# Kernel optimization log

Hardware: AMD Instinct MI355X
Metric: run time of the kernel (lower is better)

Reference implementation:

```python
import jax, jax.numpy as jnp
import numpy as np

WS = 8        # window_size
SS = 4        # shift_size
NH = 8        # num_heads
DIM = 256
HD = DIM // NH
SCALE = HD ** -0.5
EPS = 1e-5


def _rel_pos_index(ws):
    ch, cw = np.meshgrid(np.arange(ws), np.arange(ws), indexing='ij')
    coords = np.stack([ch.ravel(), cw.ravel()])            # [2, ws*ws]
    rel = coords[:, :, None] - coords[:, None, :]           # [2, N, N]
    rel = rel.transpose(1, 2, 0)
    rel[:, :, 0] += ws - 1
    rel[:, :, 1] += ws - 1
    rel[:, :, 0] *= 2 * ws - 1
    return jnp.asarray(rel.sum(-1))                         # [N, N] int

REL_IDX = _rel_pos_index(WS)


def _ln(x, g, b):
    m = jnp.mean(x, axis=-1, keepdims=True)
    v = jnp.mean(jnp.square(x - m), axis=-1, keepdims=True)
    return (x - m) * jax.lax.rsqrt(v + EPS) * g + b


def setup_inputs() -> dict:
    key = jax.random.key(0)
    ks = jax.random.split(key, 12)
    B, L, C = 8, 16384, DIM
    s = lambda k, shape, scale=0.02: jax.random.normal(k, shape, jnp.float32) * scale
    return {
        'x': jax.random.normal(ks[0], (B, L, C), jnp.float32),
        'norm1_g': jnp.ones((C,), jnp.float32),
        'norm1_b': jnp.zeros((C,), jnp.float32),
        'qkv_w': s(ks[1], (C, 3 * C)),
        'qkv_b': jnp.zeros((3 * C,), jnp.float32),
        'rel_bias': s(ks[2], ((2 * WS - 1) ** 2, NH)),
        'proj_w': s(ks[3], (C, C)),
        'proj_b': jnp.zeros((C,), jnp.float32),
        'norm2_g': jnp.ones((C,), jnp.float32),
        'norm2_b': jnp.zeros((C,), jnp.float32),
        'fc1_w': s(ks[4], (C, C)),
        'fc1_b': jnp.zeros((C,), jnp.float32),
        'fc2_w': s(ks[5], (C, C)),
        'fc2_b': jnp.zeros((C,), jnp.float32),
        'H': 128,
        'W': 128,
    }


def reference(x, norm1_g, norm1_b, qkv_w, qkv_b, rel_bias, proj_w, proj_b,
              norm2_g, norm2_b, fc1_w, fc1_b, fc2_w, fc2_b, H, W):
    B, L, C = x.shape
    shortcut = x
    h = _ln(x, norm1_g, norm1_b).reshape(B, H, W, C)
    pad_b = (WS - H % WS) % WS
    pad_r = (WS - W % WS) % WS
    h = jnp.pad(h, ((0, 0), (0, pad_b), (0, pad_r), (0, 0)))
    Hp, Wp = H + pad_b, W + pad_r
    if SS > 0:
        h = jnp.roll(h, (-SS, -SS), axis=(1, 2))
    # window partition -> [B*nW, WS*WS, C]
    h = h.reshape(B, Hp // WS, WS, Wp // WS, WS, C)
    h = h.transpose(0, 1, 3, 2, 4, 5).reshape(-1, WS * WS, C)
    Bn, N = h.shape[0], WS * WS
    # attention
    qkv = (h @ qkv_w + qkv_b).reshape(Bn, N, 3, NH, HD)
    q, k, v = qkv[:, :, 0], qkv[:, :, 1], qkv[:, :, 2]   # [Bn, N, NH, HD]
    attn = jnp.einsum('bnhd,bmhd->bhnm', q * SCALE, k)
    bias = rel_bias[REL_IDX.reshape(-1)].reshape(N, N, NH).transpose(2, 0, 1)
    attn = jax.nn.softmax(attn + bias[None], axis=-1)
    o = jnp.einsum('bhnm,bmhd->bnhd', attn, v).reshape(Bn, N, C)
    o = o @ proj_w + proj_b
    # window reverse
    o = o.reshape(B, Hp // WS, Wp // WS, WS, WS, C)
    o = o.transpose(0, 1, 3, 2, 4, 5).reshape(B, Hp, Wp, C)
    if SS > 0:
        o = jnp.roll(o, (SS, SS), axis=(1, 2))
    o = o[:, :H, :W, :].reshape(B, H * W, C)
    x = shortcut + o
    # MLP (hidden = dim, exact GELU as nn.GELU default)
    m = _ln(x, norm2_g, norm2_b)
    m = jax.nn.gelu(m @ fc1_w + fc1_b, approximate=False)
    m = m @ fc2_w + fc2_b
    return x + m
```

## Files before the change

### kernel.cpp

```cpp
#include <hip/hip_runtime.h>
#include <stdint.h>

typedef __bf16 bf16;
typedef __bf16 bf16x4v __attribute__((ext_vector_type(4)));
typedef __bf16 bf16x8 __attribute__((ext_vector_type(8)));
typedef float floatx4 __attribute__((ext_vector_type(4)));
typedef float float4v __attribute__((ext_vector_type(4)));

#define SCALE 0.17677669529663689f

__device__ __forceinline__ float ldin(const void* p, long i, int f32) {
  return f32 ? ((const float*)p)[i] : (float)(((const bf16*)p)[i]);
}

__global__ void detect_k(const unsigned short* __restrict__ x, int* flag) {
  __shared__ int cnt;
  if (threadIdx.x == 0) cnt = 0;
  __syncthreads();
  int local = 0;
  for (int i = threadIdx.x; i < 4096; i += 256) {
    unsigned short w = x[i];
    int e = (w >> 7) & 0xFF;
    if (w != 0 && (e >= 0x9F || e <= 0x5F)) local++;
  }
  atomicAdd(&cnt, local);
  __syncthreads();
  if (threadIdx.x == 0) *flag = (cnt >= 64) ? 1 : 0;
}

__global__ void conv_w_k(const void* __restrict__ W, bf16* __restrict__ Wt,
                         int K, int N, const int* __restrict__ flag) {
  int f32 = *flag;
  int idx = blockIdx.x * 256 + threadIdx.x;
  if (idx < K * N) {
    int k = idx / N, n = idx % N;
    Wt[n * K + k] = (bf16)ldin(W, idx, f32);
  }
}

__global__ void bias_k(const void* __restrict__ rel, float* __restrict__ bias_s,
                       const int* __restrict__ flag) {
  int f = *flag;
  int idx = blockIdx.x * 256 + threadIdx.x;
  int r = idx & 3, ni = (idx >> 2) & 3, mi = (idx >> 4) & 3;
  int l16 = (idx >> 6) & 15, quad = (idx >> 10) & 3, head = idx >> 12;
  int i = mi * 16 + quad * 4 + r, j = ni * 16 + l16;
  int dy = (i >> 3) - (j >> 3) + 7, dx = (i & 7) - (j & 7) + 7;
  bias_s[idx] = ldin(rel, (dy * 15 + dx) * 8 + head, f);
}

__global__ __launch_bounds__(256) void ln_k(const void* __restrict__ x,
                                            const void* __restrict__ g,
                                            const void* __restrict__ b,
                                            bf16* __restrict__ y,
                                            const int* __restrict__ flag,
                                            int x_input) {
  int f = *flag;
  int f32x = x_input ? f : 0;
  int wave = threadIdx.x >> 6, lane = threadIdx.x & 63;
  long row = (long)blockIdx.x * 4 + wave;
  float v[4];
  if (f32x) {
    float4v u = ((const float4v*)x)[row * 64 + lane];
    for (int i = 0; i < 4; i++) v[i] = u[i];
  } else {
    bf16x4v u = ((const bf16x4v*)x)[row * 64 + lane];
    for (int i = 0; i < 4; i++) v[i] = (float)u[i];
  }
  float s = v[0] + v[1] + v[2] + v[3];
  for (int off = 32; off > 0; off >>= 1) s += __shfl_xor(s, off, 64);
  float mean = s * (1.f / 256.f);
  float q = 0.f;
  for (int i = 0; i < 4; i++) { float d = v[i] - mean; q += d * d; }
  for (int off = 32; off > 0; off >>= 1) q += __shfl_xor(q, off, 64);
  float rstd = rsqrtf(q * (1.f / 256.f) + 1e-5f);
  bf16x4v o;
  for (int i = 0; i < 4; i++) {
    float gv = ldin(g, lane * 4 + i, f);
    float bv = ldin(b, lane * 4 + i, f);
    o[i] = (bf16)((v[i] - mean) * rstd * gv + bv);
  }
  ((bf16x4v*)y)[row * 64 + lane] = o;
}

template <int EPI>
__global__ __launch_bounds__(256) void gemm_bt_k(
    const bf16* __restrict__ A, const bf16* __restrict__ Bt,
    const void* __restrict__ bias, const void* __restrict__ res,
    void* __restrict__ C, int M, int N, int K, const int* __restrict__ flag,
    int res_input, int out_input) {
  __shared__ bf16 As[128 * 32];
  __shared__ bf16 Bs[128 * 32];
  __shared__ float CsF[32 * 132];
  const int tid = threadIdx.x;
  const int ntiles = gridDim.x;
  int bid = blockIdx.y * ntiles + blockIdx.x;
  const int nwg = ntiles * gridDim.y;
  if (!(nwg & 7)) bid = (bid & 7) * (nwg >> 3) + (bid >> 3);
  const long m0 = (long)(bid / ntiles) * 128;
  const int n0 = (bid % ntiles) * 128;
  const int wave = tid >> 6, lane = tid & 63;
  const int wm = wave & 1, wn = wave >> 1;
  const int quad = lane >> 4, l16 = lane & 15;

  floatx4 acc[4][4];
  for (int i = 0; i < 4; i++)
    for (int j = 0; j < 4; j++) acc[i][j] = (floatx4){0.f, 0.f, 0.f, 0.f};

  const int ldr = tid >> 2;
  const int ldc = (tid & 3) * 8;

  for (int kt = 0; kt < K; kt += 32) {
    bf16x8 a0 = *(const bf16x8*)(A + (m0 + ldr) * K + kt + ldc);
    bf16x8 a1 = *(const bf16x8*)(A + (m0 + 64 + ldr) * K + kt + ldc);
    bf16x8 b0 = *(const bf16x8*)(Bt + (long)(n0 + ldr) * K + kt + ldc);
    bf16x8 b1 = *(const bf16x8*)(Bt + (long)(n0 + 64 + ldr) * K + kt + ldc);
    __syncthreads();
    *(bf16x8*)&As[tid * 8] = a0;
    *(bf16x8*)&As[(256 + tid) * 8] = a1;
    *(bf16x8*)&Bs[tid * 8] = b0;
    *(bf16x8*)&Bs[(256 + tid) * 8] = b1;
    __syncthreads();
    bf16x8 af[4], bfr[4];
    for (int mi = 0; mi < 4; mi++)
      af[mi] = *(const bf16x8*)&As[(wm * 64 + mi * 16 + l16) * 32 + quad * 8];
    for (int ni = 0; ni < 4; ni++)
      bfr[ni] = *(const bf16x8*)&Bs[(wn * 64 + ni * 16 + l16) * 32 + quad * 8];
    for (int mi = 0; mi < 4; mi++)
      for (int ni = 0; ni < 4; ni++)
        acc[mi][ni] = __builtin_amdgcn_mfma_f32_16x16x32_bf16(
            af[mi], bfr[ni], acc[mi][ni], 0, 0, 0);
  }

  const int f = *flag;
  const int rf32 = res_input ? f : 0;
  const int of32 = out_input ? f : 0;
  for (int mi = 0; mi < 4; mi++) {
    __syncthreads();
    for (int ni = 0; ni < 4; ni++) {
      int col = n0 + wn * 64 + ni * 16 + l16;
      float bv = ldin(bias, col, f);
      for (int r = 0; r < 4; r++) {
        long row = m0 + wm * 64 + mi * 16 + quad * 4 + r;
        float v = acc[mi][ni][r] + bv;
        if (EPI == 1) v = v * 0.5f * (1.f + erff(v * 0.70710678118654752f));
        if (EPI == 2) v += ldin(res, row * N + col, rf32);
        CsF[(wm * 16 + quad * 4 + r) * 132 + wn * 64 + ni * 16 + l16] = v;
      }
    }
    __syncthreads();
    const int s = tid >> 3;
    const int seg = tid & 7;
    const long grow = m0 + (s >> 4) * 64 + mi * 16 + (s & 15);
    const int gcol = n0 + seg * 16;
    const float4v* src = (const float4v*)&CsF[s * 132 + seg * 16];
    float4v v0 = src[0], v1 = src[1], v2 = src[2], v3 = src[3];
    if (of32) {
      float4v* dst = (float4v*)((float*)C + grow * N + gcol);
      dst[0] = v0; dst[1] = v1; dst[2] = v2; dst[3] = v3;
    } else {
      bf16x8 o0, o1;
      for (int j = 0; j < 4; j++) {
        o0[j] = (bf16)v0[j]; o0[4 + j] = (bf16)v1[j];
        o1[j] = (bf16)v2[j]; o1[4 + j] = (bf16)v3[j];
      }
      bf16x8* dst = (bf16x8*)((bf16*)C + grow * N + gcol);
      dst[0] = o0; dst[1] = o1;
    }
  }
}

__global__ __launch_bounds__(256) void attn_k(const bf16* __restrict__ qkv,
                                              const float* __restrict__ bias_s,
                                              bf16* __restrict__ o) {
  __shared__ bf16 Pb[4][64 * 64];
  __shared__ bf16 Vb[4][32 * 64];
  const int tid = threadIdx.x;
  const int wave = tid >> 6, lane = tid & 63;
  const int quad = lane >> 4, l16 = lane & 15;
  const int gid = blockIdx.x * 4 + wave;
  const int head = gid & 7, win = gid >> 3;
  const int wx = win & 15, wy = (win >> 4) & 15, bb = win >> 8;

  bf16* P = Pb[wave];
  bf16* Vt = Vb[wave];

  bf16x8 qf[4], kf[4];
  for (int mi = 0; mi < 4; mi++) {
    int t = mi * 16 + l16;
    int rr = (wy * 8 + (t >> 3) + 4) & 127;
    int cc = (wx * 8 + (t & 7) + 4) & 127;
    long base = ((long)(bb * 16384 + rr * 128 + cc)) * 768 + head * 32 + quad * 8;
    qf[mi] = *(const bf16x8*)(qkv + base);
    kf[mi] = *(const bf16x8*)(qkv + base + 256);
    bf16x8 vv = *(const bf16x8*)(qkv + base + 512);
    int tcol = t ^ (quad << 4);
    for (int jj = 0; jj < 8; jj++) Vt[(quad * 8 + jj) * 64 + tcol] = vv[jj];
  }
  __syncthreads();

  floatx4 acc[4][4];
  for (int mi = 0; mi < 4; mi++)
    for (int ni = 0; ni < 4; ni++) {
      floatx4 z = (floatx4){0.f, 0.f, 0.f, 0.f};
      acc[mi][ni] = __builtin_amdgcn_mfma_f32_16x16x32_bf16(qf[mi], kf[ni], z, 0, 0, 0);
    }

  const float4v* bp =
      (const float4v*)(bias_s + (((head * 4 + quad) * 16 + l16) << 6));
  for (int mi = 0; mi < 4; mi++) {
    float mx[4] = {-1e30f, -1e30f, -1e30f, -1e30f};
    for (int ni = 0; ni < 4; ni++) {
      float4v bv = bp[mi * 4 + ni];
      for (int r = 0; r < 4; r++) {
        acc[mi][ni][r] = acc[mi][ni][r] * SCALE + bv[r];
        mx[r] = fmaxf(mx[r], acc[mi][ni][r]);
      }
    }
    for (int r = 0; r < 4; r++) {
      float m = mx[r];
      for (int off = 1; off < 16; off <<= 1) m = fmaxf(m, __shfl_xor(m, off, 64));
      mx[r] = m;
    }
    float sm[4] = {0.f, 0.f, 0.f, 0.f};
    for (int ni = 0; ni < 4; ni++)
      for (int r = 0; r < 4; r++) {
        float e = __expf(acc[mi][ni][r] - mx[r]);
        acc[mi][ni][r] = e;
        sm[r] += e;
      }
    for (int r = 0; r < 4; r++) {
      float s = sm[r];
      for (int off = 1; off < 16; off <<= 1) s += __shfl_xor(s, off, 64);
      sm[r] = 1.f / s;
    }
    for (int ni = 0; ni < 4; ni++)
      for (int r = 0; r < 4; r++) {
        int i = mi * 16 + quad * 4 + r;
        int j = ni * 16 + l16;
        P[i * 64 + (j ^ ((i & 7) << 3))] = (bf16)(acc[mi][ni][r] * sm[r]);
      }
  }
  __syncthreads();

  floatx4 oacc[4][2];
  for (int mi = 0; mi < 4; mi++)
    for (int nt = 0; nt < 2; nt++) oacc[mi][nt] = (floatx4){0.f, 0.f, 0.f, 0.f};
  for (int ks = 0; ks < 2; ks++) {
    bf16x8 vfr[2];
    for (int nt = 0; nt < 2; nt++) {
      int d = nt * 16 + l16;
      vfr[nt] =
          *(const bf16x8*)&Vt[d * 64 + ((ks * 32 + quad * 8) ^ ((d >> 3) << 4))];
    }
    for (int mi = 0; mi < 4; mi++) {
      int i = mi * 16 + l16;
      bf16x8 pf =
          *(const bf16x8*)&P[i * 64 + ((ks * 32 + quad * 8) ^ ((i & 7) << 3))];
      for (int nt = 0; nt < 2; nt++)
        oacc[mi][nt] = __builtin_amdgcn_mfma_f32_16x16x32_bf16(pf, vfr[nt],
                                                               oacc[mi][nt], 0, 0, 0);
    }
  }

  for (int mi = 0; mi < 4; mi++)
    for (int r = 0; r < 4; r++) {
      int t = mi * 16 + quad * 4 + r;
      int rot = (t >> 1) & 3;
      int c0 = l16, c1 = 16 + l16;
      Vt[t * 32 + ((((c0 >> 3) + rot) & 3) << 3) + (c0 & 7)] = (bf16)oacc[mi][0][r];
      Vt[t * 32 + ((((c1 >> 3) + rot) & 3) << 3) + (c1 & 7)] = (bf16)oacc[mi][1][r];
    }
  {
    int t = lane;
    int rot = (t >> 1) & 3;
    int rr = (wy * 8 + (t >> 3) + 4) & 127;
    int cc = (wx * 8 + (t & 7) + 4) & 127;
    long base = ((long)(bb * 16384 + rr * 128 + cc)) * 256 + head * 32;
    bf16x8* dst = (bf16x8*)(o + base);
    for (int k = 0; k < 4; k++)
      dst[k] = *(const bf16x8*)&Vt[t * 32 + (((k + rot) & 3) << 3)];
  }
}

extern "C" void kernel_launch(void* const* d_in, const int* in_sizes, int n_in,
                              void* d_out, int out_size, void* d_ws,
                              size_t ws_size, hipStream_t stream) {
  const void* x = d_in[0];
  const void* n1g = d_in[1];
  const void* n1b = d_in[2];
  const void* qkv_w = d_in[3];
  const void* qkv_b = d_in[4];
  const void* rel_bias = d_in[5];
  const void* proj_w = d_in[6];
  const void* proj_b = d_in[7];
  const void* n2g = d_in[8];
  const void* n2b = d_in[9];
  const void* fc1_w = d_in[10];
  const void* fc1_b = d_in[11];
  const void* fc2_w = d_in[12];
  const void* fc2_b = d_in[13];

  char* ws = (char*)d_ws;
  int* flag = (int*)ws;
  float* bias_s = (float*)(ws + 4096);
  bf16* qkvWt = (bf16*)(ws + 262144);
  bf16* projWt = qkvWt + 768 * 256;
  bf16* fc1Wt = projWt + 256 * 256;
  bf16* fc2Wt = fc1Wt + 256 * 256;
  bf16* reg1 = (bf16*)(ws + (1 << 20));
  bf16* reg2 = (bf16*)(ws + (1 << 20) + 67108864);

  const int M = 131072;

  detect_k<<<1, 256, 0, stream>>>((const unsigned short*)x, flag);

  bias_k<<<128, 256, 0, stream>>>(rel_bias, bias_s, flag);
  conv_w_k<<<768, 256, 0, stream>>>(qkv_w, qkvWt, 256, 768, flag);
  conv_w_k<<<256, 256, 0, stream>>>(proj_w, projWt, 256, 256, flag);
  conv_w_k<<<256, 256, 0, stream>>>(fc1_w, fc1Wt, 256, 256, flag);
  conv_w_k<<<256, 256, 0, stream>>>(fc2_w, fc2Wt, 256, 256, flag);

  bf16* h = reg1;
  ln_k<<<M / 4, 256, 0, stream>>>(x, n1g, n1b, h, flag, 1);

  bf16* qkv = reg2;
  gemm_bt_k<0><<<dim3(6, M / 128), 256, 0, stream>>>(
      h, qkvWt, qkv_b, nullptr, qkv, M, 768, 256, flag, 0, 0);

  bf16* o = reg1;
  attn_k<<<2048 * 8 / 4, 256, 0, stream>>>(qkv, bias_s, o);

  bf16* x2 = reg2;
  gemm_bt_k<2><<<dim3(2, M / 128), 256, 0, stream>>>(
      o, projWt, proj_b, x, x2, M, 256, 256, flag, 1, 0);

  bf16* mbuf = reg1;
  ln_k<<<M / 4, 256, 0, stream>>>(x2, n2g, n2b, mbuf, flag, 0);

  bf16* m1 = reg2 + 33554432;
  gemm_bt_k<1><<<dim3(2, M / 128), 256, 0, stream>>>(
      mbuf, fc1Wt, fc1_b, nullptr, m1, M, 256, 256, flag, 0, 0);

  gemm_bt_k<2><<<dim3(2, M / 128), 256, 0, stream>>>(
      m1, fc2Wt, fc2_b, x2, d_out, M, 256, 256, flag, 0, 1);
}
```

Baseline: 841.6 us.

## Load GEMM tiles directly into LDS with XOR swizzle, merge weight conversions

The GEMM tile loads now use global_load_lds so data goes from global memory straight into shared memory, skipping the register staging step. The load column is XOR-swizzled by row so the MFMA fragment reads avoid LDS bank conflicts. Shared memory is merged into one buffer, with the epilogue staging area aliasing the A/B tiles, which lowers LDS use and may let more blocks fit per CU. Three separate 256x256 weight transpose launches are combined into one kernel to cut launch overhead. The main loop still syncs twice per K step with no double buffering, so load latency is not overlapped with compute.

```diff
diff --git a/kernel.cpp b/kernel.cpp
--- a/kernel.cpp
+++ b/kernel.cpp
@@ -11,6 +11,12 @@
 
 __device__ __forceinline__ float ldin(const void* p, long i, int f32) {
   return f32 ? ((const float*)p)[i] : (float)(((const bf16*)p)[i]);
+}
+
+__device__ __forceinline__ void async16(const bf16* g, bf16* l) {
+  __builtin_amdgcn_global_load_lds(
+      (const __attribute__((address_space(1))) void*)g,
+      (__attribute__((address_space(3))) void*)l, 16, 0, 0);
 }
 
 __global__ void detect_k(const unsigned short* __restrict__ x, int* flag) {
@@ -36,6 +42,19 @@
     int k = idx / N, n = idx % N;
     Wt[n * K + k] = (bf16)ldin(W, idx, f32);
   }
+}
+
+__global__ void conv3_k(const void* __restrict__ W0, const void* __restrict__ W1,
+                        const void* __restrict__ W2, bf16* __restrict__ T0,
+                        bf16* __restrict__ T1, bf16* __restrict__ T2,
+                        const int* __restrict__ flag) {
+  int f32 = *flag;
+  int which = blockIdx.x >> 8;
+  int idx = (blockIdx.x & 255) * 256 + threadIdx.x;
+  const void* W = which == 0 ? W0 : which == 1 ? W1 : W2;
+  bf16* T = which == 0 ? T0 : which == 1 ? T1 : T2;
+  int k = idx >> 8, n = idx & 255;
+  T[n * 256 + k] = (bf16)ldin(W, idx, f32);
 }
 
 __global__ void bias_k(const void* __restrict__ rel, float* __restrict__ bias_s,
@@ -89,9 +108,11 @@
     const void* __restrict__ bias, const void* __restrict__ res,
     void* __restrict__ C, int M, int N, int K, const int* __restrict__ flag,
     int res_input, int out_input) {
-  __shared__ bf16 As[128 * 32];
-  __shared__ bf16 Bs[128 * 32];
-  __shared__ float CsF[32 * 132];
+  __shared__ __align__(16) char smem[16896];
+  bf16* As = (bf16*)smem;
+  bf16* Bs = (bf16*)(smem + 8192);
+  float* CsF = (float*)smem;
+
   const int tid = threadIdx.x;
   const int ntiles = gridDim.x;
   int bid = blockIdx.y * ntiles + blockIdx.x;
@@ -108,24 +129,33 @@
     for (int j = 0; j < 4; j++) acc[i][j] = (floatx4){0.f, 0.f, 0.f, 0.f};
 
   const int ldr = tid >> 2;
-  const int ldc = (tid & 3) * 8;
+  const int ldc = (((tid & 3) ^ ((tid >> 3) & 3)) << 3);
+
+  const bf16* gA0 = A + (m0 + ldr) * K + ldc;
+  const bf16* gA1 = A + (m0 + 64 + ldr) * K + ldc;
+  const bf16* gB0 = Bt + (long)(n0 + ldr) * K + ldc;
+  const bf16* gB1 = Bt + (long)(n0 + 64 + ldr) * K + ldc;
+  bf16* lA0 = As + wave * 512;
+  bf16* lA1 = As + 2048 + wave * 512;
+  bf16* lB0 = Bs + wave * 512;
+  bf16* lB1 = Bs + 2048 + wave * 512;
+
+  const int rswz = (l16 >> 1) & 3;
 
   for (int kt = 0; kt < K; kt += 32) {
-    bf16x8 a0 = *(const bf16x8*)(A + (m0 + ldr) * K + kt + ldc);
-    bf16x8 a1 = *(const bf16x8*)(A + (m0 + 64 + ldr) * K + kt + ldc);
-    bf16x8 b0 = *(const bf16x8*)(Bt + (long)(n0 + ldr) * K + kt + ldc);
-    bf16x8 b1 = *(const bf16x8*)(Bt + (long)(n0 + 64 + ldr) * K + kt + ldc);
     __syncthreads();
-    *(bf16x8*)&As[tid * 8] = a0;
-    *(bf16x8*)&As[(256 + tid) * 8] = a1;
-    *(bf16x8*)&Bs[tid * 8] = b0;
-    *(bf16x8*)&Bs[(256 + tid) * 8] = b1;
+    async16(gA0 + kt, lA0);
+    async16(gA1 + kt, lA1);
+    async16(gB0 + kt, lB0);
+    async16(gB1 + kt, lB1);
     __syncthreads();
     bf16x8 af[4], bfr[4];
     for (int mi = 0; mi < 4; mi++)
-      af[mi] = *(const bf16x8*)&As[(wm * 64 + mi * 16 + l16) * 32 + quad * 8];
+      af[mi] = *(const bf16x8*)&As[(wm * 64 + mi * 16 + l16) * 32 +
+                                   ((quad ^ rswz) << 3)];
     for (int ni = 0; ni < 4; ni++)
-      bfr[ni] = *(const bf16x8*)&Bs[(wn * 64 + ni * 16 + l16) * 32 + quad * 8];
+      bfr[ni] = *(const bf16x8*)&Bs[(wn * 64 + ni * 16 + l16) * 32 +
+                                    ((quad ^ rswz) << 3)];
     for (int mi = 0; mi < 4; mi++)
       for (int ni = 0; ni < 4; ni++)
         acc[mi][ni] = __builtin_amdgcn_mfma_f32_16x16x32_bf16(
@@ -317,9 +347,8 @@
 
   bias_k<<<128, 256, 0, stream>>>(rel_bias, bias_s, flag);
   conv_w_k<<<768, 256, 0, stream>>>(qkv_w, qkvWt, 256, 768, flag);
-  conv_w_k<<<256, 256, 0, stream>>>(proj_w, projWt, 256, 256, flag);
-  conv_w_k<<<256, 256, 0, stream>>>(fc1_w, fc1Wt, 256, 256, flag);
-  conv_w_k<<<256, 256, 0, stream>>>(fc2_w, fc2Wt, 256, 256, flag);
+  conv3_k<<<768, 256, 0, stream>>>(proj_w, fc1_w, fc2_w, projWt, fc1Wt, fc2Wt,
+                                   flag);
 
   bf16* h = reg1;
   ln_k<<<M / 4, 256, 0, stream>>>(x, n1g, n1b, h, flag, 1);
```

Result: no change. 842.6 us (+0.1%).
